# Kernel optimization log

Measured on AMD Instinct MI355X. Metric: run time of the kernel, lower is better.

## Reference

```python
import jax, jax.numpy as jnp
import numpy as np

B, T, H = 4, 2048, 1024
DFF = 4 * H
MAX_DEPTH = 4
TARGET_DEPTH = 2.5
BUDGET_WEIGHT = 0.01
ACT_TAU = 0.99


def setup_inputs() -> dict:
    key = jax.random.key(0)
    ks = jax.random.split(key, 6)
    s = 0.02
    return {
        "x": jax.random.normal(ks[0], (B, T, H), dtype=jnp.float32),
        "Wb1": jax.random.normal(ks[1], (H, DFF), dtype=jnp.float32) * s,
        "bb1": jnp.zeros((DFF,), dtype=jnp.float32),
        "Wb2": jax.random.normal(ks[2], (DFF, H), dtype=jnp.float32) * s,
        "bb2": jnp.zeros((H,), dtype=jnp.float32),
        "Rw1": jax.random.normal(ks[3], (MAX_DEPTH - 1, H + 1, H // 2), dtype=jnp.float32) * s,
        "Rb1": jnp.zeros((MAX_DEPTH - 1, H // 2), dtype=jnp.float32),
        "Rw2": jax.random.normal(ks[4], (MAX_DEPTH - 1, H // 2, 1), dtype=jnp.float32) * s,
        "Rb2": jnp.zeros((MAX_DEPTH - 1, 1), dtype=jnp.float32),
    }


def _body(x, Wb1, bb1, Wb2, bb2):
    # transformer-style FFN body, exact (erf) GELU to match torch nn.GELU
    h = jax.nn.gelu(jnp.einsum("btd,df->btf", x, Wb1) + bb1, approximate=False)
    return jnp.einsum("btf,fd->btd", h, Wb2) + bb2


def reference(x, Wb1, bb1, Wb2, bb2, Rw1, Rb1, Rw2, Rb2):
    # mandatory first pass
    x = _body(x, Wb1, bb1, Wb2, bb2)
    lead = x.shape[:-1]  # (B, T)
    weight_sum = jnp.ones(lead, dtype=x.dtype)
    cumulative_p = jnp.zeros(lead, dtype=x.dtype)
    still_running = jnp.ones(lead, dtype=x.dtype)
    for i in range(MAX_DEPTH - 1):
        # router: concat spike-rate feature (zeros: no scalar aux from body)
        feat = jnp.concatenate([x, jnp.zeros(lead + (1,), dtype=x.dtype)], axis=-1)
        h = jax.nn.gelu(jnp.einsum("btf,fm->btm", feat, Rw1[i]) + Rb1[i], approximate=False)
        logit = (jnp.einsum("btm,mo->bto", h, Rw2[i]) + Rb2[i])[..., 0]
        p = jax.nn.sigmoid(logit)
        # ACT remainder trick
        remainder = jnp.clip(1.0 - cumulative_p, 0.0)
        would_halt = cumulative_p + p >= ACT_TAU
        weight = jnp.where(would_halt, remainder, p) * still_running
        # soft depth mix
        x_new = _body(x, Wb1, bb1, Wb2, bb2)
        w = weight[..., None]
        x = w * x_new + (1.0 - w) * x
        weight_sum = weight_sum + weight
        cumulative_p = cumulative_p + weight
        still_running = still_running * (~would_halt).astype(x.dtype)
    avg_depth = weight_sum.mean()
    budget_loss = BUDGET_WEIGHT * jnp.square(jax.nn.relu(avg_depth - TARGET_DEPTH))
    return x, budget_loss
```

## Files before the change

kernel.cpp:

```cpp
#include <hip/hip_runtime.h>
#include <hip/hip_bf16.h>
#include <math.h>

typedef __bf16 bf16_t;
typedef __attribute__((ext_vector_type(8))) __bf16 bf16x8;
typedef __attribute__((ext_vector_type(4))) __bf16 bf16x4;
typedef __attribute__((ext_vector_type(4))) float f32x4;

#define NTOK 8192
#define HDIM 1024
#define DFF  4096
#define RHID 512

__device__ __forceinline__ float gelu_exact(float v) {
  return 0.5f * v * (1.0f + erff(v * 0.70710678118654752f));
}

__device__ __forceinline__ float gelu_fast(float v) {
  const float g = 1.5957691216057308f * (v + 0.044715f * v * v * v);
  return v / (1.0f + __expf(-g));
}

__device__ __forceinline__ void async_cp16(void* lds, const void* g) {
  __builtin_amdgcn_global_load_lds(
      (__attribute__((address_space(1))) void*)g,
      (__attribute__((address_space(3))) void*)lds, 16, 0, 0);
}

__device__ __forceinline__ void remap_tile(int g, int& mt, int& nt) {
  mt = ((g & 7) << 3) | ((g >> 3) & 7);
  nt = g >> 6;
}

template<int MODE, bool WRITE_OUT, int WM, int WN>
__device__ __forceinline__ void body_tile(
    int mt, int nt,
    const bf16_t* __restrict__ A, const bf16_t* __restrict__ Bt,
    const float* __restrict__ bias, int N, int K,
    bf16_t* __restrict__ Hout, float* __restrict__ Xout,
    bf16_t* __restrict__ Xb, bf16_t* __restrict__ Xlo,
    const float* __restrict__ Wmix,
    bf16_t* As, bf16_t* Bs)
{
  constexpr int BM  = WM * 32;
  constexpr int BN  = WN * 32;
  constexpr int ACH = BM / 32;
  constexpr int BCH = BN / 32;
  const int tid  = threadIdx.x;
  const int lane = tid & 63;
  const int wv   = tid >> 6;
  const int wm   = wv >> 1;
  const int wn   = wv & 1;
  const int lr   = lane & 15;
  const int quad = lane >> 4;
  const int m0 = mt * BM;
  const int n0 = nt * BN;

  f32x4 acc[WM][WN];
#pragma unroll
  for (int i = 0; i < WM; ++i)
#pragma unroll
    for (int j = 0; j < WN; ++j)
      acc[i][j] = (f32x4){0.f, 0.f, 0.f, 0.f};

  const int c   = tid;
  const int row = c >> 3;
  const int ks  = (((c & 7) - (row & 7)) & 7) * 8;
  const bf16_t* Agb = A  + (size_t)(m0 + row) * K + ks;
  const bf16_t* Bgb = Bt + (size_t)(n0 + row) * K + ks;
  char* lAb = (char*)As + c * 16;
  char* lBb = (char*)Bs + c * 16;

  for (int kb = 0; kb < K; kb += 64) {
    __syncthreads();
#pragma unroll
    for (int t = 0; t < ACH; ++t)
      async_cp16(lAb + 4096 * t, Agb + (size_t)32 * t * K + kb);
#pragma unroll
    for (int t = 0; t < BCH; ++t)
      async_cp16(lBb + 4096 * t, Bgb + (size_t)32 * t * K + kb);
    __syncthreads();
#pragma unroll
    for (int kk = 0; kk < 2; ++kk) {
      const int kg = kk * 4 + quad;
      bf16x8 af[WM], bfr[WN];
#pragma unroll
      for (int i = 0; i < WM; ++i) {
        const int ra = wm * (WM * 16) + i * 16 + lr;
        af[i] = *(const bf16x8*)&As[ra * 64 + ((kg + ra) & 7) * 8];
      }
#pragma unroll
      for (int j = 0; j < WN; ++j) {
        const int rb = wn * (WN * 16) + j * 16 + lr;
        bfr[j] = *(const bf16x8*)&Bs[rb * 64 + ((kg + rb) & 7) * 8];
      }
#pragma unroll
      for (int i = 0; i < WM; ++i)
#pragma unroll
        for (int j = 0; j < WN; ++j)
          acc[i][j] = __builtin_amdgcn_mfma_f32_16x16x32_bf16(af[i], bfr[j], acc[i][j], 0, 0, 0);
    }
  }

#pragma unroll
  for (int i = 0; i < WM; ++i) {
#pragma unroll
    for (int r = 0; r < 4; ++r) {
      const int gm = m0 + wm * (WM * 16) + i * 16 + quad * 4 + r;
      float wmix = 0.f, onemw = 0.f;
      if (MODE == 2) { wmix = Wmix[gm]; onemw = 1.f - wmix; }
#pragma unroll
      for (int j = 0; j < WN; ++j) {
        const int gn = n0 + wn * (WN * 16) + j * 16 + lr;
        float v = acc[i][j][r] + bias[gn];
        if (MODE == 0) {
          Hout[(size_t)gm * N + gn] = (bf16_t)gelu_fast(v);
        } else {
          const size_t idx = (size_t)gm * N + gn;
          if (MODE == 2) {
            const float xold = (float)Xb[idx] + (float)Xlo[idx];
            v = wmix * v + onemw * xold;
          }
          const bf16_t hi = (bf16_t)v;
          Xb[idx]  = hi;
          Xlo[idx] = (bf16_t)(v - (float)hi);
          if (WRITE_OUT) Xout[idx] = v;
        }
      }
    }
  }
}

__device__ __forceinline__ void router_tile(
    int mt, int nt,
    const bf16_t* __restrict__ Ah, const bf16_t* __restrict__ Al,
    const bf16_t* __restrict__ Bh, const bf16_t* __restrict__ Bl,
    const float* __restrict__ bias, float* __restrict__ Hr,
    bf16_t* Ahs, bf16_t* Als, bf16_t* Bhs, bf16_t* Bls)
{
  const int K = HDIM, N = RHID;
  const int tid  = threadIdx.x;
  const int lane = tid & 63;
  const int wv   = tid >> 6;
  const int wm   = wv >> 1;
  const int wn   = wv & 1;
  const int lr   = lane & 15;
  const int quad = lane >> 4;
  const int m0 = mt * 128;
  const int n0 = nt * 128;

  f32x4 acc[4][4];
#pragma unroll
  for (int i = 0; i < 4; ++i)
#pragma unroll
    for (int j = 0; j < 4; ++j)
      acc[i][j] = (f32x4){0.f, 0.f, 0.f, 0.f};

  const int c0 = tid;
  const int c1 = tid + 256;
  const int r0 = c0 >> 2, r1 = c1 >> 2;
  const int ks0 = ((c0 ^ r0) & 3) * 8;
  const int ks1 = ((c1 ^ r1) & 3) * 8;
  const size_t aoff0 = (size_t)(m0 + r0) * K + ks0;
  const size_t aoff1 = (size_t)(m0 + r1) * K + ks1;
  const size_t boff0 = (size_t)(n0 + r0) * K + ks0;
  const size_t boff1 = (size_t)(n0 + r1) * K + ks1;
  const int sw = ((quad ^ lr) & 3) * 8;

  for (int k0 = 0; k0 < K; k0 += 32) {
    __syncthreads();
    async_cp16((char*)Ahs + c0 * 16, Ah + aoff0 + k0);
    async_cp16((char*)Ahs + c1 * 16, Ah + aoff1 + k0);
    async_cp16((char*)Als + c0 * 16, Al + aoff0 + k0);
    async_cp16((char*)Als + c1 * 16, Al + aoff1 + k0);
    async_cp16((char*)Bhs + c0 * 16, Bh + boff0 + k0);
    async_cp16((char*)Bhs + c1 * 16, Bh + boff1 + k0);
    async_cp16((char*)Bls + c0 * 16, Bl + boff0 + k0);
    async_cp16((char*)Bls + c1 * 16, Bl + boff1 + k0);
    __syncthreads();
    bf16x8 ah[4], al[4], bh[4], bl[4];
#pragma unroll
    for (int i = 0; i < 4; ++i) {
      const int ao = (wm * 64 + i * 16 + lr) * 32 + sw;
      ah[i] = *(const bf16x8*)&Ahs[ao];
      al[i] = *(const bf16x8*)&Als[ao];
    }
#pragma unroll
    for (int j = 0; j < 4; ++j) {
      const int bo = (wn * 64 + j * 16 + lr) * 32 + sw;
      bh[j] = *(const bf16x8*)&Bhs[bo];
      bl[j] = *(const bf16x8*)&Bls[bo];
    }
#pragma unroll
    for (int i = 0; i < 4; ++i)
#pragma unroll
      for (int j = 0; j < 4; ++j) {
        acc[i][j] = __builtin_amdgcn_mfma_f32_16x16x32_bf16(ah[i], bh[j], acc[i][j], 0, 0, 0);
        acc[i][j] = __builtin_amdgcn_mfma_f32_16x16x32_bf16(al[i], bh[j], acc[i][j], 0, 0, 0);
        acc[i][j] = __builtin_amdgcn_mfma_f32_16x16x32_bf16(ah[i], bl[j], acc[i][j], 0, 0, 0);
      }
  }

#pragma unroll
  for (int i = 0; i < 4; ++i)
#pragma unroll
    for (int r = 0; r < 4; ++r) {
      const int gm = m0 + wm * 64 + i * 16 + quad * 4 + r;
#pragma unroll
      for (int j = 0; j < 4; ++j) {
        const int gn = n0 + wn * 64 + j * 16 + lr;
        Hr[(size_t)gm * N + gn] = gelu_exact(acc[i][j][r] + bias[gn]);
      }
    }
}

template<int MODE, bool WRITE_OUT>
__global__ __launch_bounds__(256, 4)
void k_gemm(const bf16_t* __restrict__ A, const bf16_t* __restrict__ Bt,
            const float* __restrict__ bias, int N, int K,
            float* __restrict__ Xout, bf16_t* __restrict__ Xb,
            bf16_t* __restrict__ Xlo, const float* __restrict__ Wmix)
{
  __shared__ __align__(16) bf16_t sm[16384];
  int mt, nt;
  remap_tile(blockIdx.x, mt, nt);
  body_tile<MODE, WRITE_OUT, 4, 4>(mt, nt, A, Bt, bias, N, K,
                                   nullptr, Xout, Xb, Xlo, Wmix, sm, sm + 8192);
}

__global__ __launch_bounds__(256, 4)
void k_body0_router(const bf16_t* __restrict__ xb, const bf16_t* __restrict__ W1t,
                    const float* __restrict__ bb1, bf16_t* __restrict__ hbuf,
                    const bf16_t* __restrict__ xlo,
                    const bf16_t* __restrict__ R1h, const bf16_t* __restrict__ R1l,
                    const float* __restrict__ Rb1, float* __restrict__ hr,
                    int nbody)
{
  __shared__ __align__(16) bf16_t sm[16384];
  const int g = blockIdx.x;
  if (g < nbody) {
    int mt, nt;
    remap_tile(g, mt, nt);
    body_tile<0, false, 4, 4>(mt, nt, xb, W1t, bb1, DFF, HDIM, hbuf,
                              nullptr, nullptr, nullptr, nullptr,
                              sm, sm + 8192);
  } else {
    int mt, nt;
    remap_tile(g - nbody, mt, nt);
    router_tile(mt, nt, xb, xlo, R1h, R1l, Rb1, hr,
                sm, sm + 4096, sm + 8192, sm + 12288);
  }
}

__global__ void act_kernel(const float* __restrict__ Hr,
                           const float* __restrict__ rw2, const float* __restrict__ rb2,
                           float* __restrict__ cum_p, float* __restrict__ still_r,
                           float* __restrict__ wsum, float* __restrict__ wvec)
{
  const int t = blockIdx.x * 4 + (threadIdx.x >> 6);
  const int lane = threadIdx.x & 63;
  float s = 0.f;
#pragma unroll
  for (int j = 0; j < 8; ++j) {
    const int m = lane + j * 64;
    s += Hr[(size_t)t * RHID + m] * rw2[m];
  }
  for (int off = 32; off > 0; off >>= 1) s += __shfl_down(s, off, 64);
  if (lane == 0) {
    const float logit = s + rb2[0];
    const float p = 1.f / (1.f + expf(-logit));
    const float cum = cum_p[t];
    const float still = still_r[t];
    const float rem = fmaxf(1.f - cum, 0.f);
    const bool halt = (cum + p) >= 0.99f;
    const float w = (halt ? rem : p) * still;
    wvec[t] = w;
    wsum[t] += w;
    cum_p[t] = cum + w;
    if (halt) still_r[t] = 0.f;
  }
}

__device__ __forceinline__ void transpose_tile(
    const float* __restrict__ src, int srcld, int dstld,
    bf16_t* __restrict__ dst, bf16_t* __restrict__ dlo,
    int bx, int by, float* tile )
{
  const int tx = threadIdx.x & 31;
  const int ty = threadIdx.x >> 5;
#pragma unroll
  for (int l = 0; l < 4; ++l)
    tile[(ty + l * 8) * 33 + tx] = src[(size_t)(by * 32 + ty + l * 8) * srcld + bx * 32 + tx];
  __syncthreads();
#pragma unroll
  for (int l = 0; l < 4; ++l) {
    const int c = bx * 32 + ty + l * 8;
    const int r = by * 32 + tx;
    const float v = tile[tx * 33 + ty + l * 8];
    const bf16_t hi = (bf16_t)v;
    dst[(size_t)c * dstld + r] = hi;
    if (dlo) dlo[(size_t)c * dstld + r] = (bf16_t)(v - (float)hi);
  }
}

__global__ void prep_kernel(const float* __restrict__ x,
                            const float* __restrict__ Wb1,
                            const float* __restrict__ Wb2,
                            const float* __restrict__ Rw1,
                            bf16_t* __restrict__ xb,
                            bf16_t* __restrict__ W1t, bf16_t* __restrict__ W2t,
                            bf16_t* __restrict__ R1h, bf16_t* __restrict__ R1l,
                            float* __restrict__ cum0, float* __restrict__ stil0,
                            float* __restrict__ wsum0)
{
  __shared__ float tile[32 * 33];
  const int g = blockIdx.x;
  if (g < 4096) {
    transpose_tile(Wb1, DFF, HDIM, W1t, nullptr, g & 127, g >> 7, tile);
  } else if (g < 8192) {
    const int g2 = g - 4096;
    transpose_tile(Wb2, HDIM, DFF, W2t, nullptr, g2 & 31, g2 >> 5, tile);
  } else if (g < 9728) {
    const int g3 = g - 8192;
    const int i  = g3 >> 9;
    const int r  = g3 & 511;
    transpose_tile(Rw1 + (size_t)i * 1025 * RHID, RHID, HDIM,
                   R1h + (size_t)i * RHID * HDIM, R1l + (size_t)i * RHID * HDIM,
                   r & 15, r >> 4, tile);
  } else if (g < 17920) {
    const int i = (g - 9728) * 256 + threadIdx.x;
    const float4 v = ((const float4*)x)[i];
    bf16x4 hb;
    hb[0] = (bf16_t)v.x; hb[1] = (bf16_t)v.y; hb[2] = (bf16_t)v.z; hb[3] = (bf16_t)v.w;
    ((bf16x4*)xb)[i] = hb;
  } else {
    const int t = (g - 17920) * 256 + threadIdx.x;
    cum0[t] = 0.f; stil0[t] = 1.f; wsum0[t] = 1.f;
  }
}

__global__ void finalize_kernel(const float* __restrict__ wsum, float* __restrict__ out)
{
  __shared__ float red[256];
  float s = 0.f;
  for (int i = threadIdx.x; i < NTOK; i += 256) s += wsum[i];
  red[threadIdx.x] = s;
  __syncthreads();
  for (int o = 128; o > 0; o >>= 1) {
    if (threadIdx.x < o) red[threadIdx.x] += red[threadIdx.x + o];
    __syncthreads();
  }
  if (threadIdx.x == 0) {
    const float avg = red[0] / (float)NTOK;
    float d = avg - 2.5f;
    d = fmaxf(d, 0.f);
    out[0] = 0.01f * d * d;
  }
}

extern "C" void kernel_launch(void* const* d_in, const int* in_sizes, int n_in,
                              void* d_out, int out_size, void* d_ws, size_t ws_size,
                              hipStream_t stream) {
  const float* x   = (const float*)d_in[0];
  const float* Wb1 = (const float*)d_in[1];
  const float* bb1 = (const float*)d_in[2];
  const float* Wb2 = (const float*)d_in[3];
  const float* bb2 = (const float*)d_in[4];
  const float* Rw1 = (const float*)d_in[5];
  const float* Rb1 = (const float*)d_in[6];
  const float* Rw2 = (const float*)d_in[7];
  const float* Rb2 = (const float*)d_in[8];
  float* out = (float*)d_out;

  char* ws = (char*)d_ws;
  size_t off = 0;
  auto carve = [&](size_t bytes) -> void* {
    void* p = ws + off;
    off += (bytes + 255) & ~(size_t)255;
    return p;
  };
  bf16_t* xb   = (bf16_t*)carve((size_t)NTOK * HDIM * 2);
  bf16_t* xlo  = (bf16_t*)carve((size_t)NTOK * HDIM * 2);
  bf16_t* hbuf = (bf16_t*)carve((size_t)NTOK * DFF * 2);
  bf16_t* W1t  = (bf16_t*)carve((size_t)HDIM * DFF * 2);
  bf16_t* W2t  = (bf16_t*)carve((size_t)HDIM * DFF * 2);
  bf16_t* R1h  = (bf16_t*)carve((size_t)3 * RHID * HDIM * 2);
  bf16_t* R1l  = (bf16_t*)carve((size_t)3 * RHID * HDIM * 2);
  float*  hr   = (float*)carve((size_t)NTOK * RHID * 4);
  float*  cum  = (float*)carve((size_t)NTOK * 4);
  float*  stil = (float*)carve((size_t)NTOK * 4);
  float*  wsum = (float*)carve((size_t)NTOK * 4);
  float*  wvec = (float*)carve((size_t)NTOK * 4);

  prep_kernel<<<17952, 256, 0, stream>>>(x, Wb1, Wb2, Rw1, xb, W1t, W2t,
                                         R1h, R1l, cum, stil, wsum);

  k_body0_router<<<2048, 256, 0, stream>>>(xb, W1t, bb1, hbuf, xlo,
                                           nullptr, nullptr, nullptr, nullptr, 2048);
  k_gemm<1, false><<<512, 256, 0, stream>>>(hbuf, W2t, bb2, HDIM, DFF,
                                            nullptr, xb, xlo, nullptr);

  for (int i = 0; i < 3; ++i) {
    k_body0_router<<<2048 + 256, 256, 0, stream>>>(
        xb, W1t, bb1, hbuf, xlo,
        R1h + (size_t)i * RHID * HDIM, R1l + (size_t)i * RHID * HDIM,
        Rb1 + (size_t)i * RHID, hr, 2048);
    act_kernel<<<2048, 256, 0, stream>>>(hr, Rw2 + (size_t)i * RHID, Rb2 + i,
                                         cum, stil, wsum, wvec);
    if (i < 2)
      k_gemm<2, false><<<512, 256, 0, stream>>>(hbuf, W2t, bb2, HDIM, DFF,
                                                nullptr, xb, xlo, wvec);
    else
      k_gemm<2, true><<<512, 256, 0, stream>>>(hbuf, W2t, bb2, HDIM, DFF,
                                               out, xb, xlo, wvec);
  }

  finalize_kernel<<<1, 256, 0, stream>>>(wsum, out + (size_t)NTOK * HDIM);
  (void)in_sizes; (void)n_in; (void)out_size; (void)ws_size;
}
```

Baseline: 868.1 us.

## Use 256x256 double-buffered 8-wave tiles for first FFN GEMM with router

Replaces the 128x128 256-thread tile for the first FFN GEMM (x·W1 + GELU) with a 256x256 tile run by 512 threads. It uses 128 KB of LDS as two buffers, loads with global_load_lds, and interleaves quarter-tile loads with MFMA phases under explicit waitcnt, barrier and setprio control. The router tile is adapted to 8 waves in the same launch. The aim is more operand reuse per LDS byte and less global traffic, with prefetch overlapping compute. The cost is far lower occupancy, only 512 body blocks, and router blocks now using 512 threads with a large LDS reservation.

New measurement: 883.0 us. About the same (+1.7%).

```diff
diff --git a/kernel.cpp b/kernel.cpp
--- a/kernel.cpp
+++ b/kernel.cpp
@@ -30,6 +30,182 @@
 __device__ __forceinline__ void remap_tile(int g, int& mt, int& nt) {
   mt = ((g & 7) << 3) | ((g >> 3) & 7);
   nt = g >> 6;
+}
+
+__device__ __forceinline__ void body_tile256(
+    int mt, int nt,
+    const bf16_t* __restrict__ A, const bf16_t* __restrict__ Bt,
+    const float* __restrict__ bias, bf16_t* __restrict__ Hout,
+    int N, int K, char* sm)
+{
+  const int tid  = threadIdx.x;
+  const int lane = tid & 63;
+  const int wv   = tid >> 6;
+  const int wm   = wv >> 2;
+  const int wn   = wv & 3;
+  const int lr   = lane & 15;
+  const int quad = lane >> 4;
+  const int m0 = mt * 256;
+  const int n0 = nt * 256;
+
+  char* const Ab0 = sm;
+  char* const Bb0 = sm + 32768;
+  char* const Ab1 = sm + 65536;
+  char* const Bb1 = sm + 98304;
+
+  const int sw0 = ((quad ^ (lr & 7)) << 4);
+  const int sw1 = (((quad + 4) ^ (lr & 7)) << 4);
+  const int aRowB = (wm * 64 + lr) << 7;
+  const int bRowB = (wn * 32 + lr) << 7;
+
+  f32x4 acc[8][4];
+#pragma unroll
+  for (int i = 0; i < 8; ++i)
+#pragma unroll
+    for (int j = 0; j < 4; ++j)
+      acc[i][j] = (f32x4){0.f, 0.f, 0.f, 0.f};
+
+  const int srow = tid >> 3;
+  const int seo  = (((tid & 7) ^ (srow & 7)) << 3);
+  const bf16_t* const aS00 = A + (size_t)(m0 +       srow) * K + seo;
+  const bf16_t* const aS01 = A + (size_t)(m0 + 128 + srow) * K + seo;
+  const bf16_t* const aS10 = A + (size_t)(m0 +  64 + srow) * K + seo;
+  const bf16_t* const aS11 = A + (size_t)(m0 + 192 + srow) * K + seo;
+  const int bc0 = ((srow >> 5) << 6) + (srow & 31);
+  const bf16_t* const bS00 = Bt + (size_t)(n0 +       bc0) * K + seo;
+  const bf16_t* const bS01 = Bt + (size_t)(n0 + 128 + bc0) * K + seo;
+  const bf16_t* const bS10 = Bt + (size_t)(n0 +  32 + bc0) * K + seo;
+  const bf16_t* const bS11 = Bt + (size_t)(n0 + 160 + bc0) * K + seo;
+  const int dst = tid << 4;
+
+  async_cp16(Ab0 + dst,                aS00);
+  async_cp16(Ab0 + dst + 8192,         aS01);
+  async_cp16(Bb0 + dst,                bS00);
+  async_cp16(Bb0 + dst + 8192,         bS01);
+  async_cp16(Ab0 + 16384 + dst,        aS10);
+  async_cp16(Ab0 + 16384 + dst + 8192, aS11);
+  async_cp16(Bb0 + 16384 + dst,        bS10);
+  async_cp16(Bb0 + 16384 + dst + 8192, bS11);
+  asm volatile("s_waitcnt vmcnt(4)" ::: "memory");
+  __builtin_amdgcn_s_barrier();
+
+  bf16x8 a0[4], a1[4], b00[2], b01[2], b10[2], b11[2];
+
+  const int NT = K >> 6;
+  for (int t = 0; t < NT; ++t) {
+    char* const Ac = (t & 1) ? Ab1 : Ab0;
+    char* const Bc = (t & 1) ? Bb1 : Bb0;
+    char* const An = (t & 1) ? Ab0 : Ab1;
+    char* const Bn = (t & 1) ? Bb0 : Bb1;
+    const size_t kbn = (size_t)((t + 1 < NT) ? t + 1 : t) << 6;
+
+#pragma unroll
+    for (int i = 0; i < 4; ++i) {
+      const char* p = Ac + aRowB + i * 2048;
+      a0[i] = *(const bf16x8*)(p + sw0);
+      a1[i] = *(const bf16x8*)(p + sw1);
+    }
+#pragma unroll
+    for (int j = 0; j < 2; ++j) {
+      const char* p = Bc + bRowB + j * 2048;
+      b00[j] = *(const bf16x8*)(p + sw0);
+      b01[j] = *(const bf16x8*)(p + sw1);
+    }
+    async_cp16(An + dst,        aS00 + kbn);
+    async_cp16(An + dst + 8192, aS01 + kbn);
+    __builtin_amdgcn_s_barrier();
+    asm volatile("s_waitcnt lgkmcnt(0)" ::: "memory");
+    __builtin_amdgcn_sched_barrier(0);
+    __builtin_amdgcn_s_setprio(1);
+#pragma unroll
+    for (int i = 0; i < 4; ++i)
+#pragma unroll
+      for (int j = 0; j < 2; ++j) {
+        acc[i][j] = __builtin_amdgcn_mfma_f32_16x16x32_bf16(a0[i], b00[j], acc[i][j], 0, 0, 0);
+        acc[i][j] = __builtin_amdgcn_mfma_f32_16x16x32_bf16(a1[i], b01[j], acc[i][j], 0, 0, 0);
+      }
+    __builtin_amdgcn_s_setprio(0);
+    asm volatile("s_waitcnt vmcnt(2)" ::: "memory");
+    __builtin_amdgcn_s_barrier();
+
+#pragma unroll
+    for (int j = 0; j < 2; ++j) {
+      const char* p = Bc + 16384 + bRowB + j * 2048;
+      b10[j] = *(const bf16x8*)(p + sw0);
+      b11[j] = *(const bf16x8*)(p + sw1);
+    }
+    async_cp16(Bn + dst,        bS00 + kbn);
+    async_cp16(Bn + dst + 8192, bS01 + kbn);
+    __builtin_amdgcn_s_barrier();
+    asm volatile("s_waitcnt lgkmcnt(0)" ::: "memory");
+    __builtin_amdgcn_sched_barrier(0);
+    __builtin_amdgcn_s_setprio(1);
+#pragma unroll
+    for (int i = 0; i < 4; ++i)
+#pragma unroll
+      for (int j = 0; j < 2; ++j) {
+        acc[i][2+j] = __builtin_amdgcn_mfma_f32_16x16x32_bf16(a0[i], b10[j], acc[i][2+j], 0, 0, 0);
+        acc[i][2+j] = __builtin_amdgcn_mfma_f32_16x16x32_bf16(a1[i], b11[j], acc[i][2+j], 0, 0, 0);
+      }
+    __builtin_amdgcn_s_setprio(0);
+    __builtin_amdgcn_s_barrier();
+
+#pragma unroll
+    for (int i = 0; i < 4; ++i) {
+      const char* p = Ac + 16384 + aRowB + i * 2048;
+      a0[i] = *(const bf16x8*)(p + sw0);
+      a1[i] = *(const bf16x8*)(p + sw1);
+    }
+    async_cp16(An + 16384 + dst,        aS10 + kbn);
+    async_cp16(An + 16384 + dst + 8192, aS11 + kbn);
+    __builtin_amdgcn_s_barrier();
+    asm volatile("s_waitcnt lgkmcnt(0)" ::: "memory");
+    __builtin_amdgcn_sched_barrier(0);
+    __builtin_amdgcn_s_setprio(1);
+#pragma unroll
+    for (int i = 0; i < 4; ++i)
+#pragma unroll
+      for (int j = 0; j < 2; ++j) {
+        acc[4+i][2+j] = __builtin_amdgcn_mfma_f32_16x16x32_bf16(a0[i], b10[j], acc[4+i][2+j], 0, 0, 0);
+        acc[4+i][2+j] = __builtin_amdgcn_mfma_f32_16x16x32_bf16(a1[i], b11[j], acc[4+i][2+j], 0, 0, 0);
+      }
+    __builtin_amdgcn_s_setprio(0);
+    __builtin_amdgcn_s_barrier();
+
+    async_cp16(Bn + 16384 + dst,        bS10 + kbn);
+    async_cp16(Bn + 16384 + dst + 8192, bS11 + kbn);
+    __builtin_amdgcn_s_barrier();
+    __builtin_amdgcn_s_setprio(1);
+#pragma unroll
+    for (int i = 0; i < 4; ++i)
+#pragma unroll
+      for (int j = 0; j < 2; ++j) {
+        acc[4+i][j] = __builtin_amdgcn_mfma_f32_16x16x32_bf16(a0[i], b00[j], acc[4+i][j], 0, 0, 0);
+        acc[4+i][j] = __builtin_amdgcn_mfma_f32_16x16x32_bf16(a1[i], b01[j], acc[4+i][j], 0, 0, 0);
+      }
+    __builtin_amdgcn_s_setprio(0);
+    asm volatile("s_waitcnt vmcnt(4)" ::: "memory");
+    __builtin_amdgcn_s_barrier();
+  }
+  asm volatile("s_waitcnt vmcnt(0)" ::: "memory");
+
+#pragma unroll
+  for (int mh = 0; mh < 2; ++mh)
+#pragma unroll
+    for (int i = 0; i < 4; ++i)
+#pragma unroll
+      for (int r = 0; r < 4; ++r) {
+        const int gm = m0 + wm * 128 + mh * 64 + i * 16 + quad * 4 + r;
+        bf16_t* const orow = Hout + (size_t)gm * N + n0 + wn * 64 + lr;
+#pragma unroll
+        for (int nh = 0; nh < 2; ++nh)
+#pragma unroll
+          for (int j = 0; j < 2; ++j) {
+            const int cn = nh * 32 + j * 16;
+            const float v = acc[mh * 4 + i][nh * 2 + j][r] + bias[n0 + wn * 64 + cn + lr];
+            orow[cn] = (bf16_t)gelu_fast(v);
+          }
+      }
 }
 
 template<int MODE, bool WRITE_OUT, int WM, int WN>
@@ -131,7 +307,7 @@
   }
 }
 
-__device__ __forceinline__ void router_tile(
+__device__ __forceinline__ void router_tile512(
     int mt, int nt,
     const bf16_t* __restrict__ Ah, const bf16_t* __restrict__ Al,
     const bf16_t* __restrict__ Bh, const bf16_t* __restrict__ Bl,
@@ -142,43 +318,35 @@
   const int tid  = threadIdx.x;
   const int lane = tid & 63;
   const int wv   = tid >> 6;
-  const int wm   = wv >> 1;
-  const int wn   = wv & 1;
+  const int wm   = wv >> 2;
+  const int wn   = wv & 3;
   const int lr   = lane & 15;
   const int quad = lane >> 4;
   const int m0 = mt * 128;
   const int n0 = nt * 128;
 
-  f32x4 acc[4][4];
+  f32x4 acc[4][2];
 #pragma unroll
   for (int i = 0; i < 4; ++i)
 #pragma unroll
-    for (int j = 0; j < 4; ++j)
+    for (int j = 0; j < 2; ++j)
       acc[i][j] = (f32x4){0.f, 0.f, 0.f, 0.f};
 
-  const int c0 = tid;
-  const int c1 = tid + 256;
-  const int r0 = c0 >> 2, r1 = c1 >> 2;
-  const int ks0 = ((c0 ^ r0) & 3) * 8;
-  const int ks1 = ((c1 ^ r1) & 3) * 8;
-  const size_t aoff0 = (size_t)(m0 + r0) * K + ks0;
-  const size_t aoff1 = (size_t)(m0 + r1) * K + ks1;
-  const size_t boff0 = (size_t)(n0 + r0) * K + ks0;
-  const size_t boff1 = (size_t)(n0 + r1) * K + ks1;
-  const int sw = ((quad ^ lr) & 3) * 8;
+  const int r   = tid >> 2;
+  const int ks  = ((tid ^ r) & 3) * 8;
+  const size_t aoff = (size_t)(m0 + r) * K + ks;
+  const size_t boff = (size_t)(n0 + r) * K + ks;
+  const int dst = tid << 4;
+  const int sw  = ((quad ^ lr) & 3) * 8;
 
   for (int k0 = 0; k0 < K; k0 += 32) {
     __syncthreads();
-    async_cp16((char*)Ahs + c0 * 16, Ah + aoff0 + k0);
-    async_cp16((char*)Ahs + c1 * 16, Ah + aoff1 + k0);
-    async_cp16((char*)Als + c0 * 16, Al + aoff0 + k0);
-    async_cp16((char*)Als + c1 * 16, Al + aoff1 + k0);
-    async_cp16((char*)Bhs + c0 * 16, Bh + boff0 + k0);
-    async_cp16((char*)Bhs + c1 * 16, Bh + boff1 + k0);
-    async_cp16((char*)Bls + c0 * 16, Bl + boff0 + k0);
-    async_cp16((char*)Bls + c1 * 16, Bl + boff1 + k0);
+    async_cp16((char*)Ahs + dst, Ah + aoff + k0);
+    async_cp16((char*)Als + dst, Al + aoff + k0);
+    async_cp16((char*)Bhs + dst, Bh + boff + k0);
+    async_cp16((char*)Bls + dst, Bl + boff + k0);
     __syncthreads();
-    bf16x8 ah[4], al[4], bh[4], bl[4];
+    bf16x8 ah[4], al[4], bh[2], bl[2];
 #pragma unroll
     for (int i = 0; i < 4; ++i) {
       const int ao = (wm * 64 + i * 16 + lr) * 32 + sw;
@@ -186,15 +354,15 @@
       al[i] = *(const bf16x8*)&Als[ao];
     }
 #pragma unroll
-    for (int j = 0; j < 4; ++j) {
-      const int bo = (wn * 64 + j * 16 + lr) * 32 + sw;
+    for (int j = 0; j < 2; ++j) {
+      const int bo = (wn * 32 + j * 16 + lr) * 32 + sw;
       bh[j] = *(const bf16x8*)&Bhs[bo];
       bl[j] = *(const bf16x8*)&Bls[bo];
     }
 #pragma unroll
     for (int i = 0; i < 4; ++i)
 #pragma unroll
-      for (int j = 0; j < 4; ++j) {
+      for (int j = 0; j < 2; ++j) {
         acc[i][j] = __builtin_amdgcn_mfma_f32_16x16x32_bf16(ah[i], bh[j], acc[i][j], 0, 0, 0);
         acc[i][j] = __builtin_amdgcn_mfma_f32_16x16x32_bf16(al[i], bh[j], acc[i][j], 0, 0, 0);
         acc[i][j] = __builtin_amdgcn_mfma_f32_16x16x32_bf16(ah[i], bl[j], acc[i][j], 0, 0, 0);
@@ -204,12 +372,12 @@
 #pragma unroll
   for (int i = 0; i < 4; ++i)
 #pragma unroll
-    for (int r = 0; r < 4; ++r) {
-      const int gm = m0 + wm * 64 + i * 16 + quad * 4 + r;
-#pragma unroll
-      for (int j = 0; j < 4; ++j) {
-        const int gn = n0 + wn * 64 + j * 16 + lr;
-        Hr[(size_t)gm * N + gn] = gelu_exact(acc[i][j][r] + bias[gn]);
+    for (int rr = 0; rr < 4; ++rr) {
+      const int gm = m0 + wm * 64 + i * 16 + quad * 4 + rr;
+#pragma unroll
+      for (int j = 0; j < 2; ++j) {
+        const int gn = n0 + wn * 32 + j * 16 + lr;
+        Hr[(size_t)gm * N + gn] = gelu_exact(acc[i][j][rr] + bias[gn]);
       }
     }
 }
@@ -228,27 +396,25 @@
                                    nullptr, Xout, Xb, Xlo, Wmix, sm, sm + 8192);
 }
 
-__global__ __launch_bounds__(256, 4)
-void k_body0_router(const bf16_t* __restrict__ xb, const bf16_t* __restrict__ W1t,
-                    const float* __restrict__ bb1, bf16_t* __restrict__ hbuf,
-                    const bf16_t* __restrict__ xlo,
-                    const bf16_t* __restrict__ R1h, const bf16_t* __restrict__ R1l,
-                    const float* __restrict__ Rb1, float* __restrict__ hr,
-                    int nbody)
-{
-  __shared__ __align__(16) bf16_t sm[16384];
+__global__ __launch_bounds__(512, 2)
+void k_body256_router(const bf16_t* __restrict__ xb, const bf16_t* __restrict__ W1t,
+                      const float* __restrict__ bb1, bf16_t* __restrict__ hbuf,
+                      const bf16_t* __restrict__ xlo,
+                      const bf16_t* __restrict__ R1h, const bf16_t* __restrict__ R1l,
+                      const float* __restrict__ Rb1, float* __restrict__ hr,
+                      int nbody)
+{
+  __shared__ __align__(128) char sm[131072];
   const int g = blockIdx.x;
   if (g < nbody) {
-    int mt, nt;
-    remap_tile(g, mt, nt);
-    body_tile<0, false, 4, 4>(mt, nt, xb, W1t, bb1, DFF, HDIM, hbuf,
-                              nullptr, nullptr, nullptr, nullptr,
-                              sm, sm + 8192);
+    const int wgid = ((g & 7) << 6) | (g >> 3);
+    body_tile256(wgid & 31, wgid >> 5, xb, W1t, bb1, hbuf, DFF, HDIM, sm);
   } else {
     int mt, nt;
     remap_tile(g - nbody, mt, nt);
-    router_tile(mt, nt, xb, xlo, R1h, R1l, Rb1, hr,
-                sm, sm + 4096, sm + 8192, sm + 12288);
+    router_tile512(mt, nt, xb, xlo, R1h, R1l, Rb1, hr,
+                   (bf16_t*)sm, (bf16_t*)(sm + 8192),
+                   (bf16_t*)(sm + 16384), (bf16_t*)(sm + 24576));
   }
 }
 
@@ -395,16 +561,16 @@
   prep_kernel<<<17952, 256, 0, stream>>>(x, Wb1, Wb2, Rw1, xb, W1t, W2t,
                                          R1h, R1l, cum, stil, wsum);
 
-  k_body0_router<<<2048, 256, 0, stream>>>(xb, W1t, bb1, hbuf, xlo,
-                                           nullptr, nullptr, nullptr, nullptr, 2048);
+  k_body256_router<<<512, 512, 0, stream>>>(xb, W1t, bb1, hbuf, xlo,
+                                            nullptr, nullptr, nullptr, nullptr, 512);
   k_gemm<1, false><<<512, 256, 0, stream>>>(hbuf, W2t, bb2, HDIM, DFF,
                                             nullptr, xb, xlo, nullptr);
 
   for (int i = 0; i < 3; ++i) {
-    k_body0_router<<<2048 + 256, 256, 0, stream>>>(
+    k_body256_router<<<512 + 256, 512, 0, stream>>>(
         xb, W1t, bb1, hbuf, xlo,
         R1h + (size_t)i * RHID * HDIM, R1l + (size_t)i * RHID * HDIM,
-        Rb1 + (size_t)i * RHID, hr, 2048);
+        Rb1 + (size_t)i * RHID, hr, 512);
     act_kernel<<<2048, 256, 0, stream>>>(hr, Rw2 + (size_t)i * RHID, Rb2 + i,
                                          cum, stil, wsum, wvec);
     if (i < 2)
```

## Compact still-running tokens for the final ACT iteration to skip halted rows

Applied to the files above, without the earlier changes.

After the second router step, the ACT kernel builds a compacted index list of tokens that are still running, using an atomic counter. The last iteration's router GEMM, FFN up-projection and down-projection gather rows through that list, and tiles beyond the active count exit early. Halted tokens get their final output from a new copy-out kernel. The aim is to skip FFN work for tokens whose mixing weight is zero. In exchange it adds an atomic list build and an extra copy pass, and the token order in the list is nondeterministic.

Result: slower. 1.014 ms (+16.8%).

```diff
diff --git a/kernel.cpp b/kernel.cpp
--- a/kernel.cpp
+++ b/kernel.cpp
@@ -32,7 +32,7 @@
   nt = g >> 6;
 }
 
-template<int MODE, bool WRITE_OUT, int WM, int WN>
+template<int MODE, bool WRITE_OUT, int WM, int WN, bool COMPACT>
 __device__ __forceinline__ void body_tile(
     int mt, int nt,
     const bf16_t* __restrict__ A, const bf16_t* __restrict__ Bt,
@@ -40,6 +40,7 @@
     bf16_t* __restrict__ Hout, float* __restrict__ Xout,
     bf16_t* __restrict__ Xb, bf16_t* __restrict__ Xlo,
     const float* __restrict__ Wmix,
+    const int* __restrict__ idxl, int cnt,
     bf16_t* As, bf16_t* Bs)
 {
   constexpr int BM  = WM * 32;
@@ -66,7 +67,13 @@
   const int c   = tid;
   const int row = c >> 3;
   const int ks  = (((c & 7) - (row & 7)) & 7) * 8;
-  const bf16_t* Agb = A  + (size_t)(m0 + row) * K + ks;
+  size_t aoff[ACH];
+#pragma unroll
+  for (int t = 0; t < ACH; ++t) {
+    int rr = m0 + row + 32 * t;
+    if (COMPACT && MODE == 0) rr = idxl[rr < cnt ? rr : cnt - 1];
+    aoff[t] = (size_t)rr * K + ks;
+  }
   const bf16_t* Bgb = Bt + (size_t)(n0 + row) * K + ks;
   char* lAb = (char*)As + c * 16;
   char* lBb = (char*)Bs + c * 16;
@@ -75,7 +82,7 @@
     __syncthreads();
 #pragma unroll
     for (int t = 0; t < ACH; ++t)
-      async_cp16(lAb + 4096 * t, Agb + (size_t)32 * t * K + kb);
+      async_cp16(lAb + 4096 * t, A + aoff[t] + kb);
 #pragma unroll
     for (int t = 0; t < BCH; ++t)
       async_cp16(lBb + 4096 * t, Bgb + (size_t)32 * t * K + kb);
@@ -107,8 +114,14 @@
 #pragma unroll
     for (int r = 0; r < 4; ++r) {
       const int gm = m0 + wm * (WM * 16) + i * 16 + quad * 4 + r;
+      bool act_row = true;
+      int tok = gm;
+      if (COMPACT && MODE == 2) {
+        act_row = gm < cnt;
+        tok = idxl[act_row ? gm : cnt - 1];
+      }
       float wmix = 0.f, onemw = 0.f;
-      if (MODE == 2) { wmix = Wmix[gm]; onemw = 1.f - wmix; }
+      if (MODE == 2) { wmix = Wmix[tok]; onemw = 1.f - wmix; }
 #pragma unroll
       for (int j = 0; j < WN; ++j) {
         const int gn = n0 + wn * (WN * 16) + j * 16 + lr;
@@ -116,26 +129,30 @@
         if (MODE == 0) {
           Hout[(size_t)gm * N + gn] = (bf16_t)gelu_fast(v);
         } else {
-          const size_t idx = (size_t)gm * N + gn;
+          const size_t idx = (size_t)tok * N + gn;
           if (MODE == 2) {
             const float xold = (float)Xb[idx] + (float)Xlo[idx];
             v = wmix * v + onemw * xold;
           }
-          const bf16_t hi = (bf16_t)v;
-          Xb[idx]  = hi;
-          Xlo[idx] = (bf16_t)(v - (float)hi);
-          if (WRITE_OUT) Xout[idx] = v;
+          if (act_row) {
+            const bf16_t hi = (bf16_t)v;
+            Xb[idx]  = hi;
+            Xlo[idx] = (bf16_t)(v - (float)hi);
+            if (WRITE_OUT) Xout[idx] = v;
+          }
         }
       }
     }
   }
 }
 
+template<bool COMPACT>
 __device__ __forceinline__ void router_tile(
     int mt, int nt,
     const bf16_t* __restrict__ Ah, const bf16_t* __restrict__ Al,
     const bf16_t* __restrict__ Bh, const bf16_t* __restrict__ Bl,
     const float* __restrict__ bias, float* __restrict__ Hr,
+    const int* __restrict__ idxl, int cnt,
     bf16_t* Ahs, bf16_t* Als, bf16_t* Bhs, bf16_t* Bls)
 {
   const int K = HDIM, N = RHID;
@@ -161,8 +178,13 @@
   const int r0 = c0 >> 2, r1 = c1 >> 2;
   const int ks0 = ((c0 ^ r0) & 3) * 8;
   const int ks1 = ((c1 ^ r1) & 3) * 8;
-  const size_t aoff0 = (size_t)(m0 + r0) * K + ks0;
-  const size_t aoff1 = (size_t)(m0 + r1) * K + ks1;
+  int tr0 = m0 + r0, tr1 = m0 + r1;
+  if (COMPACT) {
+    tr0 = idxl[tr0 < cnt ? tr0 : cnt - 1];
+    tr1 = idxl[tr1 < cnt ? tr1 : cnt - 1];
+  }
+  const size_t aoff0 = (size_t)tr0 * K + ks0;
+  const size_t aoff1 = (size_t)tr1 * K + ks1;
   const size_t boff0 = (size_t)(n0 + r0) * K + ks0;
   const size_t boff1 = (size_t)(n0 + r1) * K + ks1;
   const int sw = ((quad ^ lr) & 3) * 8;
@@ -206,56 +228,74 @@
 #pragma unroll
     for (int r = 0; r < 4; ++r) {
       const int gm = m0 + wm * 64 + i * 16 + quad * 4 + r;
+      bool act_row = true;
+      int tok = gm;
+      if (COMPACT) {
+        act_row = gm < cnt;
+        tok = idxl[act_row ? gm : cnt - 1];
+      }
 #pragma unroll
       for (int j = 0; j < 4; ++j) {
         const int gn = n0 + wn * 64 + j * 16 + lr;
-        Hr[(size_t)gm * N + gn] = gelu_exact(acc[i][j][r] + bias[gn]);
-      }
-    }
-}
-
-template<int MODE, bool WRITE_OUT>
+        if (act_row) Hr[(size_t)tok * N + gn] = gelu_exact(acc[i][j][r] + bias[gn]);
+      }
+    }
+}
+
+template<int MODE, bool WRITE_OUT, bool COMPACT>
 __global__ __launch_bounds__(256, 4)
 void k_gemm(const bf16_t* __restrict__ A, const bf16_t* __restrict__ Bt,
             const float* __restrict__ bias, int N, int K,
             float* __restrict__ Xout, bf16_t* __restrict__ Xb,
-            bf16_t* __restrict__ Xlo, const float* __restrict__ Wmix)
+            bf16_t* __restrict__ Xlo, const float* __restrict__ Wmix,
+            const int* __restrict__ idxl, const int* __restrict__ cntp)
 {
   __shared__ __align__(16) bf16_t sm[16384];
+  int cnt = NTOK;
+  if (COMPACT) cnt = *cntp;
   int mt, nt;
   remap_tile(blockIdx.x, mt, nt);
-  body_tile<MODE, WRITE_OUT, 4, 4>(mt, nt, A, Bt, bias, N, K,
-                                   nullptr, Xout, Xb, Xlo, Wmix, sm, sm + 8192);
-}
-
+  if (COMPACT && mt * 128 >= cnt) return;
+  body_tile<MODE, WRITE_OUT, 4, 4, COMPACT>(mt, nt, A, Bt, bias, N, K,
+                                            nullptr, Xout, Xb, Xlo, Wmix,
+                                            idxl, cnt, sm, sm + 8192);
+}
+
+template<bool COMPACT>
 __global__ __launch_bounds__(256, 4)
 void k_body0_router(const bf16_t* __restrict__ xb, const bf16_t* __restrict__ W1t,
                     const float* __restrict__ bb1, bf16_t* __restrict__ hbuf,
                     const bf16_t* __restrict__ xlo,
                     const bf16_t* __restrict__ R1h, const bf16_t* __restrict__ R1l,
                     const float* __restrict__ Rb1, float* __restrict__ hr,
+                    const int* __restrict__ idxl, const int* __restrict__ cntp,
                     int nbody)
 {
   __shared__ __align__(16) bf16_t sm[16384];
+  int cnt = NTOK;
+  if (COMPACT) cnt = *cntp;
   const int g = blockIdx.x;
   if (g < nbody) {
     int mt, nt;
     remap_tile(g, mt, nt);
-    body_tile<0, false, 4, 4>(mt, nt, xb, W1t, bb1, DFF, HDIM, hbuf,
-                              nullptr, nullptr, nullptr, nullptr,
-                              sm, sm + 8192);
+    if (COMPACT && mt * 128 >= cnt) return;
+    body_tile<0, false, 4, 4, COMPACT>(mt, nt, xb, W1t, bb1, DFF, HDIM, hbuf,
+                                       nullptr, nullptr, nullptr, nullptr,
+                                       idxl, cnt, sm, sm + 8192);
   } else {
     int mt, nt;
     remap_tile(g - nbody, mt, nt);
-    router_tile(mt, nt, xb, xlo, R1h, R1l, Rb1, hr,
-                sm, sm + 4096, sm + 8192, sm + 12288);
+    if (COMPACT && mt * 128 >= cnt) return;
+    router_tile<COMPACT>(mt, nt, xb, xlo, R1h, R1l, Rb1, hr, idxl, cnt,
+                         sm, sm + 4096, sm + 8192, sm + 12288);
   }
 }
 
 __global__ void act_kernel(const float* __restrict__ Hr,
                            const float* __restrict__ rw2, const float* __restrict__ rb2,
                            float* __restrict__ cum_p, float* __restrict__ still_r,
-                           float* __restrict__ wsum, float* __restrict__ wvec)
+                           float* __restrict__ wsum, float* __restrict__ wvec,
+                           int build, int* __restrict__ cntp, int* __restrict__ idxl)
 {
   const int t = blockIdx.x * 4 + (threadIdx.x >> 6);
   const int lane = threadIdx.x & 63;
@@ -278,7 +318,29 @@
     wsum[t] += w;
     cum_p[t] = cum + w;
     if (halt) still_r[t] = 0.f;
-  }
+    if (build && still > 0.f && !halt) {
+      const int pos = atomicAdd(cntp, 1);
+      idxl[pos] = t;
+    }
+  }
+}
+
+__global__ void copyout_kernel(const bf16_t* __restrict__ Xb,
+                               const bf16_t* __restrict__ Xlo,
+                               const float* __restrict__ still,
+                               float* __restrict__ Xout)
+{
+  const int e = blockIdx.x * 256 + threadIdx.x;
+  const int t = e >> 8;
+  if (still[t] != 0.f) return;
+  const bf16x4 hi = ((const bf16x4*)Xb)[e];
+  const bf16x4 lo = ((const bf16x4*)Xlo)[e];
+  float4 o;
+  o.x = (float)hi[0] + (float)lo[0];
+  o.y = (float)hi[1] + (float)lo[1];
+  o.z = (float)hi[2] + (float)lo[2];
+  o.w = (float)hi[3] + (float)lo[3];
+  ((float4*)Xout)[e] = o;
 }
 
 __device__ __forceinline__ void transpose_tile(
@@ -311,7 +373,7 @@
                             bf16_t* __restrict__ W1t, bf16_t* __restrict__ W2t,
                             bf16_t* __restrict__ R1h, bf16_t* __restrict__ R1l,
                             float* __restrict__ cum0, float* __restrict__ stil0,
-                            float* __restrict__ wsum0)
+                            float* __restrict__ wsum0, int* __restrict__ cntp)
 {
   __shared__ float tile[32 * 33];
   const int g = blockIdx.x;
@@ -336,6 +398,7 @@
   } else {
     const int t = (g - 17920) * 256 + threadIdx.x;
     cum0[t] = 0.f; stil0[t] = 1.f; wsum0[t] = 1.f;
+    if (t == 0) *cntp = 0;
   }
 }
 
@@ -391,29 +454,45 @@
   float*  stil = (float*)carve((size_t)NTOK * 4);
   float*  wsum = (float*)carve((size_t)NTOK * 4);
   float*  wvec = (float*)carve((size_t)NTOK * 4);
+  int*    idxl = (int*)carve((size_t)NTOK * 4);
+  int*    cntp = (int*)carve(256);
 
   prep_kernel<<<17952, 256, 0, stream>>>(x, Wb1, Wb2, Rw1, xb, W1t, W2t,
-                                         R1h, R1l, cum, stil, wsum);
-
-  k_body0_router<<<2048, 256, 0, stream>>>(xb, W1t, bb1, hbuf, xlo,
-                                           nullptr, nullptr, nullptr, nullptr, 2048);
-  k_gemm<1, false><<<512, 256, 0, stream>>>(hbuf, W2t, bb2, HDIM, DFF,
-                                            nullptr, xb, xlo, nullptr);
-
-  for (int i = 0; i < 3; ++i) {
-    k_body0_router<<<2048 + 256, 256, 0, stream>>>(
-        xb, W1t, bb1, hbuf, xlo,
-        R1h + (size_t)i * RHID * HDIM, R1l + (size_t)i * RHID * HDIM,
-        Rb1 + (size_t)i * RHID, hr, 2048);
-    act_kernel<<<2048, 256, 0, stream>>>(hr, Rw2 + (size_t)i * RHID, Rb2 + i,
-                                         cum, stil, wsum, wvec);
-    if (i < 2)
-      k_gemm<2, false><<<512, 256, 0, stream>>>(hbuf, W2t, bb2, HDIM, DFF,
-                                                nullptr, xb, xlo, wvec);
-    else
-      k_gemm<2, true><<<512, 256, 0, stream>>>(hbuf, W2t, bb2, HDIM, DFF,
-                                               out, xb, xlo, wvec);
-  }
+                                         R1h, R1l, cum, stil, wsum, cntp);
+
+  k_body0_router<false><<<2048, 256, 0, stream>>>(
+      xb, W1t, bb1, hbuf, xlo, nullptr, nullptr, nullptr, nullptr,
+      idxl, cntp, 2048);
+  k_gemm<1, false, false><<<512, 256, 0, stream>>>(
+      hbuf, W2t, bb2, HDIM, DFF, nullptr, xb, xlo, nullptr, idxl, cntp);
+
+  k_body0_router<false><<<2048 + 256, 256, 0, stream>>>(
+      xb, W1t, bb1, hbuf, xlo,
+      R1h, R1l, Rb1, hr, idxl, cntp, 2048);
+  act_kernel<<<2048, 256, 0, stream>>>(hr, Rw2, Rb2, cum, stil, wsum, wvec,
+                                       0, cntp, idxl);
+  k_gemm<2, false, false><<<512, 256, 0, stream>>>(
+      hbuf, W2t, bb2, HDIM, DFF, nullptr, xb, xlo, wvec, idxl, cntp);
+
+  k_body0_router<false><<<2048 + 256, 256, 0, stream>>>(
+      xb, W1t, bb1, hbuf, xlo,
+      R1h + (size_t)RHID * HDIM, R1l + (size_t)RHID * HDIM,
+      Rb1 + RHID, hr, idxl, cntp, 2048);
+  act_kernel<<<2048, 256, 0, stream>>>(hr, Rw2 + RHID, Rb2 + 1,
+                                       cum, stil, wsum, wvec, 1, cntp, idxl);
+  k_gemm<2, false, false><<<512, 256, 0, stream>>>(
+      hbuf, W2t, bb2, HDIM, DFF, nullptr, xb, xlo, wvec, idxl, cntp);
+
+  copyout_kernel<<<8192, 256, 0, stream>>>(xb, xlo, stil, out);
+
+  k_body0_router<true><<<2048 + 256, 256, 0, stream>>>(
+      xb, W1t, bb1, hbuf, xlo,
+      R1h + (size_t)2 * RHID * HDIM, R1l + (size_t)2 * RHID * HDIM,
+      Rb1 + 2 * RHID, hr, idxl, cntp, 2048);
+  act_kernel<<<2048, 256, 0, stream>>>(hr, Rw2 + 2 * RHID, Rb2 + 2,
+                                       cum, stil, wsum, wvec, 0, cntp, idxl);
+  k_gemm<2, true, true><<<512, 256, 0, stream>>>(
+      hbuf, W2t, bb2, HDIM, DFF, out, xb, xlo, wvec, idxl, cntp);
 
   finalize_kernel<<<1, 256, 0, stream>>>(wsum, out + (size_t)NTOK * HDIM);
   (void)in_sizes; (void)n_in; (void)out_size; (void)ws_size;
```
